# Performance work log

Measured on AMD Instinct MI355X. Metric: run time of the kernel, lower is better.

## Reference

```python
import jax, jax.numpy as jnp
import numpy as np

EPS = 1e-4

def setup_inputs() -> dict:
    key = jax.random.key(0)
    k1, k2 = jax.random.split(key)
    N, C, H, W = 64, 256, 56, 56
    x = jax.random.normal(k1, (N, C, H, W), dtype=jnp.float32)
    weight = jax.random.uniform(k2, (C, 1), dtype=jnp.float32)
    bias = jnp.zeros((C, 1), dtype=jnp.float32)
    return {"x": x, "weight": weight, "bias": bias}

def _zca_forward(x, weight, bias, groups=16):
    N, C, H, W = x.shape
    G = groups
    c = C // G  # per-group channel count
    M = N * H * W
    # [C, N*H*W], matching x.transpose(0,1).view(C, -1)
    xf = jnp.transpose(x, (1, 0, 2, 3)).reshape(C, M)
    mu = jnp.mean(xf, axis=1, keepdims=True)
    xc = xf - mu
    # Per-group covariance: the torch code builds the full CxC matrix and takes
    # diagonal blocks; computing only the blocks is the same math.
    xg = xc.reshape(G, c, M)
    cov = jnp.einsum('gim,gjm->gij', xg, xg) / M  # [G, c, c]
    cov = cov + EPS * jnp.eye(c, dtype=x.dtype)
    # torch.svd on a symmetric PSD matrix -> eigendecomposition; proj = V e^{-1/2} V^T
    e, v = jnp.linalg.eigh(cov)  # e: [G,c], v: [G,c,c]
    inv_sqrt = jax.lax.rsqrt(e)
    proj = jnp.einsum('gik,gk,gjk->gij', v, inv_sqrt, v)  # [G, c, c]
    xw = jnp.einsum('gij,gjm->gim', proj, xg).reshape(C, M)
    out = xw * weight + bias
    return jnp.transpose(out.reshape(C, N, H, W), (1, 0, 2, 3))

def reference(x, weight, bias):
    return _zca_forward(x, weight, bias)
```

## Files before the change

### kernel.cpp

```cpp
#include <hip/hip_runtime.h>
#include <math.h>

namespace {

constexpr int HW    = 56 * 56;
constexpr int NB    = 64;
constexpr int CTOT  = 256;
constexpr int CPG   = 16;
constexpr int GRP   = 16;
constexpr int MTOT  = NB * HW;
constexpr int NPAIR = 136;
constexpr int NACC  = CPG + NPAIR;
constexpr float EPSR = 1e-4f;
constexpr int NS_IT = 14;
constexpr int PPW   = NPAIR / 4;
constexpr int F2    = HW / 2;
constexpr int CITER = HW / 64;

__host__ __device__ constexpr int pair_idx(int i, int j) {
    return i * CPG - (i * (i - 1)) / 2 + (j - i);
}

template<int W>
__device__ __forceinline__ void accum_pairs(const float (&v)[CPG],
                                            float (&acc)[PPW], float (&sum)[4]) {
#pragma unroll
    for (int i = 0; i < CPG; ++i) {
#pragma unroll
        for (int j = i; j < CPG; ++j) {
            const int k = pair_idx(i, j);
            if (k >= W * PPW && k < (W + 1) * PPW)
                acc[k - W * PPW] = fmaf(v[i], v[j], acc[k - W * PPW]);
        }
    }
#pragma unroll
    for (int c = 0; c < 4; ++c) sum[c] += v[W * 4 + c];
}

template<int W>
__device__ __forceinline__ void writeback(float* __restrict__ dst,
                                          const float (&acc)[PPW],
                                          const float (&sum)[4]) {
#pragma unroll
    for (int k = 0; k < PPW; ++k) atomicAdd(dst + CPG + W * PPW + k, acc[k]);
#pragma unroll
    for (int c = 0; c < 4; ++c) atomicAdd(dst + W * 4 + c, sum[c]);
}

__global__ __launch_bounds__(256)
void cov_kernel(const float* __restrict__ x, float* __restrict__ accg) {
    const int bid  = blockIdx.x;
    const int g    = bid >> 6;
    const int n    = bid & (NB - 1);
    const int t    = threadIdx.x;
    const int w    = t >> 6;
    const int lane = t & 63;

    const float* xb = x + ((size_t)n * CTOT + (size_t)g * CPG) * HW;

    float acc[PPW], sum[4];
#pragma unroll
    for (int k = 0; k < PPW; ++k) acc[k] = 0.f;
#pragma unroll
    for (int c = 0; c < 4; ++c) sum[c] = 0.f;

    float v[CPG], vn[CPG];
#pragma unroll
    for (int j = 0; j < CPG; ++j) v[j] = xb[(size_t)j * HW + lane];

    for (int it = 0; it < CITER; ++it) {
        const bool more = (it + 1 < CITER);
        if (more) {
            const int hw = (it + 1) * 64 + lane;
#pragma unroll
            for (int j = 0; j < CPG; ++j) vn[j] = xb[(size_t)j * HW + hw];
        }
        if      (w == 0) accum_pairs<0>(v, acc, sum);
        else if (w == 1) accum_pairs<1>(v, acc, sum);
        else if (w == 2) accum_pairs<2>(v, acc, sum);
        else             accum_pairs<3>(v, acc, sum);
        if (!more) break;
#pragma unroll
        for (int j = 0; j < CPG; ++j) v[j] = vn[j];
    }

#pragma unroll
    for (int k = 0; k < PPW; ++k) {
#pragma unroll
        for (int s = 32; s > 0; s >>= 1) acc[k] += __shfl_xor(acc[k], s, 64);
    }
#pragma unroll
    for (int c = 0; c < 4; ++c) {
#pragma unroll
        for (int s = 32; s > 0; s >>= 1) sum[c] += __shfl_xor(sum[c], s, 64);
    }

    if (lane == 0) {
        float* dst = accg + g * NACC;
        if      (w == 0) writeback<0>(dst, acc, sum);
        else if (w == 1) writeback<1>(dst, acc, sum);
        else if (w == 2) writeback<2>(dst, acc, sum);
        else             writeback<3>(dst, acc, sum);
    }
}

__global__ __launch_bounds__(256, 1)
void ns_kernel(const float* __restrict__ accg,
               const float* __restrict__ weight, const float* __restrict__ bias,
               float* __restrict__ Pout, float* __restrict__ bfout) {
    __shared__ float A[CPG][CPG], Y[CPG][CPG], Z[CPG][CPG], T[CPG][CPG];
    __shared__ float mu[CPG];
    __shared__ float s_tr;
    const int g = blockIdx.x;
    const int t = threadIdx.x;
    const int i = t >> 4, j = t & 15;
    const float* a = accg + g * NACC;
    const float invM = 1.0f / (float)MTOT;

    if (t < CPG) mu[t] = a[t] * invM;
    __syncthreads();
    {
        const int lo = i < j ? i : j;
        const int hi = i < j ? j : i;
        float c = a[CPG + pair_idx(lo, hi)] * invM - mu[i] * mu[j];
        if (i == j) c += EPSR;
        A[i][j] = c;
    }
    __syncthreads();
    if (t == 0) {
        float tr = 0.f;
        for (int k = 0; k < CPG; ++k) tr += A[k][k];
        s_tr = tr;
    }
    __syncthreads();
    const float tr = s_tr;
    Y[i][j] = A[i][j] / tr;
    Z[i][j] = (i == j) ? 1.f : 0.f;
    __syncthreads();

    for (int it = 0; it < NS_IT; ++it) {
        float zy = 0.f;
#pragma unroll
        for (int k = 0; k < CPG; ++k) zy += Z[i][k] * Y[k][j];
        const float tij = ((i == j) ? 1.5f : 0.f) - 0.5f * zy;
        T[i][j] = tij;
        __syncthreads();
        float y2 = 0.f, z2 = 0.f;
#pragma unroll
        for (int k = 0; k < CPG; ++k) {
            y2 += Y[i][k] * T[k][j];
            z2 += T[i][k] * Z[k][j];
        }
        __syncthreads();
        Y[i][j] = y2;
        Z[i][j] = z2;
        __syncthreads();
    }

    const float pw = (Z[i][j] / sqrtf(tr)) * weight[g * CPG + i];
    Pout[g * 256 + j * CPG + i] = pw;

    T[i][j] = pw;
    __syncthreads();
    if (t < CPG) {
        float o = 0.f;
        for (int k = 0; k < CPG; ++k) o += T[t][k] * mu[k];
        bfout[g * CPG + t] = bias[g * CPG + t] - o;
    }
}

__global__ __launch_bounds__(256)
void apply_kernel(const float* __restrict__ x, const float* __restrict__ Pg,
                  const float* __restrict__ bfg, float* __restrict__ out) {
    __shared__ __align__(16) float Pl[CPG * CPG];
    __shared__ float bl[CPG];

    const int slab = blockIdx.x;
    const int g    = slab & (GRP - 1);
    const int n    = slab >> 4;
    const int t    = threadIdx.x;

    Pl[t] = Pg[g * 256 + t];
    if (t < CPG) bl[t] = bfg[g * CPG + t];
    __syncthreads();

    const size_t base = ((size_t)n * CTOT + (size_t)g * CPG) * HW;
    const float* xb = x + base;
    float*       ob = out + base;

    for (int f2 = t; f2 < F2; f2 += 256) {
        const float* px = xb + 2 * f2;
        float2 xv[CPG];
#pragma unroll
        for (int j = 0; j < CPG; ++j)
            xv[j] = *(const float2*)(px + j * HW);

        float2 acc[CPG];
#pragma unroll
        for (int i = 0; i < CPG; ++i) {
            const float bb = bl[i];
            acc[i] = make_float2(bb, bb);
        }

#pragma unroll
        for (int j = 0; j < CPG; ++j) {
            const float2 xj = xv[j];
            const float4* pc = (const float4*)&Pl[j * CPG];
#pragma unroll
            for (int q = 0; q < 4; ++q) {
                const float4 p = pc[q];
                acc[q * 4 + 0].x = fmaf(p.x, xj.x, acc[q * 4 + 0].x);
                acc[q * 4 + 0].y = fmaf(p.x, xj.y, acc[q * 4 + 0].y);
                acc[q * 4 + 1].x = fmaf(p.y, xj.x, acc[q * 4 + 1].x);
                acc[q * 4 + 1].y = fmaf(p.y, xj.y, acc[q * 4 + 1].y);
                acc[q * 4 + 2].x = fmaf(p.z, xj.x, acc[q * 4 + 2].x);
                acc[q * 4 + 2].y = fmaf(p.z, xj.y, acc[q * 4 + 2].y);
                acc[q * 4 + 3].x = fmaf(p.w, xj.x, acc[q * 4 + 3].x);
                acc[q * 4 + 3].y = fmaf(p.w, xj.y, acc[q * 4 + 3].y);
            }
        }

        float* po = ob + 2 * f2;
#pragma unroll
        for (int i = 0; i < CPG; ++i)
            *(float2*)(po + i * HW) = acc[i];
    }
}

}

extern "C" void kernel_launch(void* const* d_in, const int* in_sizes, int n_in,
                              void* d_out, int out_size, void* d_ws, size_t ws_size,
                              hipStream_t stream) {
    const float* x      = (const float*)d_in[0];
    const float* weight = (const float*)d_in[1];
    const float* bias   = (const float*)d_in[2];
    float* out = (float*)d_out;
    float* ws  = (float*)d_ws;

    float* acc = ws;
    float* Pw  = ws + 2560;
    float* bf  = ws + 6656;

    hipMemsetAsync(acc, 0, GRP * NACC * sizeof(float), stream);

    cov_kernel<<<GRP * NB, 256, 0, stream>>>(x, acc);
    ns_kernel<<<GRP, 256, 0, stream>>>(acc, weight, bias, Pw, bf);
    apply_kernel<<<NB * GRP, 256, 0, stream>>>(x, Pw, bf, out);
}
```

Measured before the change: 655.6 us.

## Stage covariance tiles into LDS with async global-to-LDS double buffering

The covariance kernel no longer has every wave redundantly load all 16 channels from global memory. Each wave now loads 4 channels of a 256-wide spatial tile into a double-buffered LDS array using global_load_lds, and all waves then read the full tile from LDS as float2. This cuts global load traffic by four times and overlaps the next tile's load with compute, at the cost of block-wide barriers and LDS use. The apply loop is also marked unroll 1, likely to limit register pressure.

```diff
diff --git a/kernel.cpp b/kernel.cpp
--- a/kernel.cpp
+++ b/kernel.cpp
@@ -15,26 +15,34 @@
 constexpr int NS_IT = 14;
 constexpr int PPW   = NPAIR / 4;
 constexpr int F2    = HW / 2;
-constexpr int CITER = HW / 64;
+constexpr int CTILE = 256;
+constexpr int NTILE = (HW + CTILE - 1) / CTILE;
 
 __host__ __device__ constexpr int pair_idx(int i, int j) {
     return i * CPG - (i * (i - 1)) / 2 + (j - i);
 }
 
+#define GLL16(src, dst)                                                        \
+    __builtin_amdgcn_global_load_lds(                                          \
+        (const __attribute__((address_space(1))) void*)(src),                  \
+        (__attribute__((address_space(3))) void*)(dst), 16, 0, 0)
+
 template<int W>
-__device__ __forceinline__ void accum_pairs(const float (&v)[CPG],
-                                            float (&acc)[PPW], float (&sum)[4]) {
+__device__ __forceinline__ void accum2(const float2 (&v)[CPG],
+                                       float (&acc)[PPW], float (&sum)[4]) {
 #pragma unroll
     for (int i = 0; i < CPG; ++i) {
 #pragma unroll
         for (int j = i; j < CPG; ++j) {
             const int k = pair_idx(i, j);
-            if (k >= W * PPW && k < (W + 1) * PPW)
-                acc[k - W * PPW] = fmaf(v[i], v[j], acc[k - W * PPW]);
-        }
-    }
-#pragma unroll
-    for (int c = 0; c < 4; ++c) sum[c] += v[W * 4 + c];
+            if (k >= W * PPW && k < (W + 1) * PPW) {
+                acc[k - W * PPW] = fmaf(v[i].x, v[j].x, acc[k - W * PPW]);
+                acc[k - W * PPW] = fmaf(v[i].y, v[j].y, acc[k - W * PPW]);
+            }
+        }
+    }
+#pragma unroll
+    for (int c = 0; c < 4; ++c) sum[c] += v[W * 4 + c].x + v[W * 4 + c].y;
 }
 
 template<int W>
@@ -49,6 +57,8 @@
 
 __global__ __launch_bounds__(256)
 void cov_kernel(const float* __restrict__ x, float* __restrict__ accg) {
+    __shared__ __align__(16) float xs[2][CPG][CTILE];
+
     const int bid  = blockIdx.x;
     const int g    = bid >> 6;
     const int n    = bid & (NB - 1);
@@ -64,24 +74,41 @@
 #pragma unroll
     for (int c = 0; c < 4; ++c) sum[c] = 0.f;
 
-    float v[CPG], vn[CPG];
-#pragma unroll
-    for (int j = 0; j < CPG; ++j) v[j] = xb[(size_t)j * HW + lane];
-
-    for (int it = 0; it < CITER; ++it) {
-        const bool more = (it + 1 < CITER);
-        if (more) {
-            const int hw = (it + 1) * 64 + lane;
-#pragma unroll
-            for (int j = 0; j < CPG; ++j) vn[j] = xb[(size_t)j * HW + hw];
-        }
-        if      (w == 0) accum_pairs<0>(v, acc, sum);
-        else if (w == 1) accum_pairs<1>(v, acc, sum);
-        else if (w == 2) accum_pairs<2>(v, acc, sum);
-        else             accum_pairs<3>(v, acc, sum);
-        if (!more) break;
-#pragma unroll
-        for (int j = 0; j < CPG; ++j) v[j] = vn[j];
+    auto stage = [&](int buf, int tile) {
+        const int pos0 = tile * CTILE;
+        const int len  = HW - pos0 < CTILE ? HW - pos0 : CTILE;
+#pragma unroll
+        for (int jj = 0; jj < 4; ++jj) {
+            const int j = w * 4 + jj;
+            if (4 * lane < len)
+                GLL16(xb + (size_t)j * HW + pos0 + 4 * lane, &xs[buf][j][0]);
+        }
+    };
+
+    stage(0, 0);
+    __syncthreads();
+
+    int cur = 0;
+    for (int tile = 0; tile < NTILE; ++tile) {
+        if (tile + 1 < NTILE) stage(cur ^ 1, tile + 1);
+        const int pos0 = tile * CTILE;
+        const int len  = HW - pos0 < CTILE ? HW - pos0 : CTILE;
+#pragma unroll
+        for (int h = 0; h < 2; ++h) {
+            const int p = h * 128 + 2 * lane;
+            if (p < len) {
+                float2 v2[CPG];
+#pragma unroll
+                for (int j = 0; j < CPG; ++j)
+                    v2[j] = *(const float2*)&xs[cur][j][p];
+                if      (w == 0) accum2<0>(v2, acc, sum);
+                else if (w == 1) accum2<1>(v2, acc, sum);
+                else if (w == 2) accum2<2>(v2, acc, sum);
+                else             accum2<3>(v2, acc, sum);
+            }
+        }
+        __syncthreads();
+        cur ^= 1;
     }
 
 #pragma unroll
@@ -188,6 +215,7 @@
     const float* xb = x + base;
     float*       ob = out + base;
 
+#pragma unroll 1
     for (int f2 = t; f2 < F2; f2 += 256) {
         const float* px = xb + 2 * f2;
         float2 xv[CPG];
```

Result: faster. 642.7 us (-2.0%).
